# Kernel optimization log

Hardware: AMD Instinct MI355X
Metric: run time of the kernel (lower is better)

Reference implementation:

```python
import jax, jax.numpy as jnp
import numpy as np

C = 64          # channels
K = 15          # sum(shell_sizes)=1+14
H = 32          # neighbors per query
N = 50000       # support points (== query points M)
RADIUS = 1.0
SIGMA = 0.7
INF = 1e6
BN_EPS = 1e-5


def _init_kernel_points(key):
    # stand-in for load_kernels: 1 center point + 14 points on a sphere shell
    pts = jax.random.normal(key, (K - 1, 3), dtype=jnp.float32)
    pts = pts / jnp.linalg.norm(pts, axis=1, keepdims=True) * RADIUS
    return jnp.concatenate([jnp.zeros((1, 3), jnp.float32), pts], axis=0)


def setup_inputs() -> dict:
    key = jax.random.key(0)
    ks = jax.random.split(key, 10)
    q_pts = jax.random.normal(ks[0], (N, 3), dtype=jnp.float32)
    s_pts = jax.random.normal(ks[1], (N, 3), dtype=jnp.float32)
    s_feats = jax.random.normal(ks[2], (N, C), dtype=jnp.float32)
    neighb_inds = jax.random.randint(ks[3], (N, H), 0, N)
    kernel_points = _init_kernel_points(ks[4])
    # alpha_mlp: Linear(C->C, no bias) -> BatchNorm -> LeakyReLU(0.1) -> Linear(C->K*C)
    lim1 = 1.0 / np.sqrt(C)
    W1 = jax.random.uniform(ks[5], (C, C), jnp.float32, -lim1, lim1)
    gamma = jnp.ones((C,), jnp.float32)
    beta = jnp.zeros((C,), jnp.float32)
    W2 = jax.random.uniform(ks[6], (C, K * C), jnp.float32, -lim1, lim1)
    b2 = jax.random.uniform(ks[7], (K * C,), jnp.float32, -lim1, lim1)
    return {"q_pts": q_pts, "s_pts": s_pts, "s_feats": s_feats,
            "neighb_inds": neighb_inds, "kernel_points": kernel_points,
            "W1": W1, "gamma": gamma, "beta": beta, "W2": W2, "b2": b2}


def reference(q_pts, s_pts, s_feats, neighb_inds, kernel_points, W1, gamma, beta, W2, b2):
    M = q_pts.shape[0]
    # alpha_mlp on pooled (= center) features: (M, C) -> (M, K*C)
    h = s_feats @ W1
    mu = jnp.mean(h, axis=0)
    var = jnp.var(h, axis=0)
    h = (h - mu) / jnp.sqrt(var + BN_EPS) * gamma + beta
    h = jax.nn.leaky_relu(h, 0.1)
    conv_weights = (h @ W2 + b2).reshape(M, K, C)

    # gather neighbor features with a zero padding row (index N -> zeros)
    padded_feats = jnp.concatenate([s_feats, jnp.zeros((1, C), s_feats.dtype)], axis=0)
    neighbor_feats = padded_feats[neighb_inds]                 # (M, H, C)

    # relative neighbor positions with inf padding point
    s_pts_pad = jnp.concatenate([s_pts, jnp.full((1, 3), INF, s_pts.dtype)], axis=0)
    neighbors = s_pts_pad[neighb_inds] - q_pts[:, None, :]     # (M, H, 3)

    # kernel-point influence: nearest kernel point + linear influence
    diff = neighbors[:, :, None, :] - kernel_points            # (M, H, K, 3)
    sq_d = jnp.sum(diff * diff, axis=-1)                       # (M, H, K)
    nn_sq = jnp.min(sq_d, axis=-1)                             # (M, H)
    nn_idx = jnp.argmin(sq_d, axis=-1)                         # (M, H)
    infl = jnp.clip(1.0 - jnp.sqrt(nn_sq) / SIGMA, 0.0)        # (M, H)

    # per-neighbor channel weights from the MLP output, gathered by 1nn kernel point
    nw = jnp.take_along_axis(conv_weights, nn_idx[:, :, None], axis=1)  # (M, H, C)
    nw = nw * infl[:, :, None]

    # weighted aggregation (merge=mul, aggr=sum over neighbors)
    return jnp.sum(neighbor_feats * nw, axis=1)                # (M, C)
```

## Files before the change

### kernel.cpp

```cpp
#include <hip/hip_runtime.h>
#include <math.h>

#define N_PTS 50000
#define CCH   64
#define KP    15
#define NH    32
#define SIGMA 0.7f
#define BN_EPS 1e-5f
#define LEAKY 0.1f
#define QB    16
#define STATS_BLOCKS 1024
#define CW_KSTRIDE_B 2176

typedef short bf16x8 __attribute__((ext_vector_type(8)));
typedef float floatx4 __attribute__((ext_vector_type(4)));

__device__ __forceinline__ unsigned short f2b(float f) {
    union { float f; unsigned u; } v; v.f = f;
    return (unsigned short)((v.u + 0x7FFFu + ((v.u >> 16) & 1u)) >> 16);
}
__device__ __forceinline__ float b2f(unsigned short b) {
    union { unsigned u; float f; } v; v.u = ((unsigned)b) << 16;
    return v.f;
}
__device__ __forceinline__ float blo(unsigned u) {
    union { unsigned u; float f; } v; v.u = u << 16;
    return v.f;
}
__device__ __forceinline__ float bhi(unsigned u) {
    union { unsigned u; float f; } v; v.u = u & 0xFFFF0000u;
    return v.f;
}
__device__ __forceinline__ unsigned cvtpk(float lo, float hi) {
    unsigned r;
    asm("v_cvt_pk_bf16_f32 %0, %1, %2" : "=v"(r) : "v"(lo), "v"(hi));
    return r;
}

__global__ __launch_bounds__(256) void k_prep(const float* __restrict__ sf,
                                              const float* __restrict__ W1,
                                              const float* __restrict__ W2,
                                              float* __restrict__ bn,
                                              unsigned short* __restrict__ hst,
                                              unsigned short* __restrict__ w2b,
                                              unsigned short* __restrict__ sfb) {
    int t = threadIdx.x;
    if (blockIdx.x >= STATS_BLOCKS) {
        int g = (blockIdx.x - STATS_BLOCKS) * 256 + t;
        int lane = g & 63, s = (g >> 6) & 1, tt = g >> 7;
        int col = lane & 15, quad = lane >> 4;
        int base = (s * 32 + quad * 8) * 960 + tt * 16 + col;
        ushort4 lo, hi;
        lo.x = f2b(W2[base + 0 * 960]); lo.y = f2b(W2[base + 1 * 960]);
        lo.z = f2b(W2[base + 2 * 960]); lo.w = f2b(W2[base + 3 * 960]);
        hi.x = f2b(W2[base + 4 * 960]); hi.y = f2b(W2[base + 5 * 960]);
        hi.z = f2b(W2[base + 6 * 960]); hi.w = f2b(W2[base + 7 * 960]);
        *(ushort4*)(w2b + g * 8)     = lo;
        *(ushort4*)(w2b + g * 8 + 4) = hi;
        return;
    }
    int c = t & 63, ml = t >> 6;
    float w1c[64];
    #pragma unroll
    for (int i = 0; i < 64; ++i) w1c[i] = W1[i * 64 + c];
    __shared__ float rows[4][64];
    float acc_s = 0.f, acc_q = 0.f;
    for (int m0 = blockIdx.x * 4; m0 < N_PTS; m0 += STATS_BLOCKS * 4) {
        __syncthreads();
        float v = sf[m0 * 64 + t];
        ((float*)rows)[t] = v;
        sfb[m0 * 64 + t] = f2b(v);
        __syncthreads();
        float h = 0.f;
        #pragma unroll
        for (int i4 = 0; i4 < 16; ++i4) {
            float4 r = *(const float4*)&rows[ml][i4 * 4];
            h += r.x * w1c[i4 * 4] + r.y * w1c[i4 * 4 + 1]
               + r.z * w1c[i4 * 4 + 2] + r.w * w1c[i4 * 4 + 3];
        }
        acc_s += h;
        acc_q += h * h;
        hst[(m0 + ml) * 64 + c] = f2b(h);
    }
    __shared__ float red[2][256];
    red[0][t] = acc_s; red[1][t] = acc_q;
    __syncthreads();
    if (t < 64) {
        float s = red[0][t] + red[0][64 + t] + red[0][128 + t] + red[0][192 + t];
        float q = red[1][t] + red[1][64 + t] + red[1][128 + t] + red[1][192 + t];
        atomicAdd(&bn[t], s);
        atomicAdd(&bn[64 + t], q);
    }
}

__global__ __launch_bounds__(256, 4) void k_main(
    const float* __restrict__ q_pts, const float* __restrict__ s_pts,
    const unsigned short* __restrict__ sfb, const int* __restrict__ nb,
    const float* __restrict__ kpts, const float* __restrict__ gamma,
    const float* __restrict__ beta, const float* __restrict__ bn,
    const float* __restrict__ b2, const unsigned short* __restrict__ w2b,
    const unsigned short* __restrict__ hst, float* __restrict__ out) {

    __shared__ __align__(16) unsigned cwP[KP * 32 * 17];
    __shared__ float abS[128];
    __shared__ int      nCnt[QB];
    __shared__ unsigned nPack[QB][NH];
    __shared__ float    nInf[QB][NH];

    int t = threadIdx.x;
    int lane = t & 63, wv = t >> 6;
    int m0 = blockIdx.x * QB;

    if (t < 64) {
        float mu  = bn[t] * (1.0f / N_PTS);
        float var = bn[64 + t] * (1.0f / N_PTS) - mu * mu;
        float a   = gamma[t] * rsqrtf(var + BN_EPS);
        abS[t]      = a;
        abS[64 + t] = beta[t] - mu * a;
    }
    ((unsigned*)nPack)[t]       = 0u;
    ((unsigned*)nPack)[t + 256] = 0u;
    ((float*)nInf)[t]           = 0.f;
    ((float*)nInf)[t + 256]     = 0.f;
    __syncthreads();

    int row = lane & 15, half = lane >> 4;
    bf16x8 r0, r1;
    {
        const unsigned short* hrow = hst + (m0 + row) * 64 + half * 8;
        r0 = *(const bf16x8*)(hrow);
        r1 = *(const bf16x8*)(hrow + 32);
    }

    float kpr[45];
    #pragma unroll
    for (int i = 0; i < 45; ++i) kpr[i] = kpts[i];

    #pragma unroll
    for (int it = 0; it < 2; ++it) {
        int task = t + 256 * it;
        int q = task >> 5, hh = task & 31;
        int m = m0 + q;
        int idx = nb[m * NH + hh];
        float px = s_pts[idx * 3 + 0] - q_pts[m * 3 + 0];
        float py = s_pts[idx * 3 + 1] - q_pts[m * 3 + 1];
        float pz = s_pts[idx * 3 + 2] - q_pts[m * 3 + 2];
        float best = 1e30f; int bi = 0;
        #pragma unroll
        for (int k = 0; k < KP; ++k) {
            float dx = px - kpr[k * 3], dy = py - kpr[k * 3 + 1], dz = pz - kpr[k * 3 + 2];
            float d = dx * dx + dy * dy + dz * dz;
            if (d < best) { best = d; bi = k; }
        }
        float infl = 1.f - sqrtf(best) * (1.0f / SIGMA);
        bool keep = infl > 0.f;
        unsigned long long bal = __ballot(keep);
        unsigned mym = (unsigned)(bal >> (lane & 32));
        int pos = __popc(mym & ((1u << (lane & 31)) - 1u));
        if (keep) {
            nPack[q][pos] = (unsigned)idx | ((unsigned)(bi * CW_KSTRIDE_B) << 16);
            nInf[q][pos]  = infl;
        }
        if ((lane & 31) == 0) nCnt[q] = __popc(mym);
    }

    bf16x8 a0, a1;
    {
        unsigned* A0 = (unsigned*)&a0;
        unsigned* A1 = (unsigned*)&a1;
        #pragma unroll
        for (int jw = 0; jw < 4; ++jw) {
            int c0 = half * 8 + jw * 2;
            float g00 = abS[c0]     * b2f((unsigned short)r0[jw * 2])     + abS[64 + c0];
            float g01 = abS[c0 + 1] * b2f((unsigned short)r0[jw * 2 + 1]) + abS[64 + c0 + 1];
            g00 = g00 > 0.f ? g00 : LEAKY * g00;
            g01 = g01 > 0.f ? g01 : LEAKY * g01;
            A0[jw] = cvtpk(g00, g01);
            int c1 = 32 + c0;
            float g10 = abS[c1]     * b2f((unsigned short)r1[jw * 2])     + abS[64 + c1];
            float g11 = abS[c1 + 1] * b2f((unsigned short)r1[jw * 2 + 1]) + abS[64 + c1 + 1];
            g10 = g10 > 0.f ? g10 : LEAKY * g10;
            g11 = g11 > 0.f ? g11 : LEAKY * g11;
            A1[jw] = cvtpk(g10, g11);
        }
    }

    {
        int colq = lane & 15, quad = lane >> 4;
        bf16x8 Lf[3], Ls[3], Mf[3], Ms[3];
        #pragma unroll
        for (int i = 0; i < 3; ++i) {
            int tt = wv * 15 + i;
            Lf[i] = *(const bf16x8*)(w2b + ((tt * 2 + 0) * 64 + lane) * 8);
            Ls[i] = *(const bf16x8*)(w2b + ((tt * 2 + 1) * 64 + lane) * 8);
        }
        #pragma unroll
        for (int g = 0; g < 5; ++g) {
            if (g < 4) {
                #pragma unroll
                for (int i = 0; i < 3; ++i) {
                    int tt = wv * 15 + (g + 1) * 3 + i;
                    Mf[i] = *(const bf16x8*)(w2b + ((tt * 2 + 0) * 64 + lane) * 8);
                    Ms[i] = *(const bf16x8*)(w2b + ((tt * 2 + 1) * 64 + lane) * 8);
                }
            }
            #pragma unroll
            for (int i = 0; i < 3; ++i) {
                int tt = wv * 15 + g * 3 + i;
                floatx4 acc = {0.f, 0.f, 0.f, 0.f};
                acc = __builtin_amdgcn_mfma_f32_16x16x32_bf16(Lf[i], a0, acc, 0, 0, 0);
                acc = __builtin_amdgcn_mfma_f32_16x16x32_bf16(Ls[i], a1, acc, 0, 0, 0);
                int n0 = tt * 16 + quad * 4;
                float4 bb = *(const float4*)&b2[n0];
                int k  = n0 >> 6;
                int c2 = (n0 & 63) >> 1;
                unsigned w0 = cvtpk(acc[0] + bb.x, acc[1] + bb.y);
                unsigned w1 = cvtpk(acc[2] + bb.z, acc[3] + bb.w);
                unsigned* dst = cwP + (k * 544 + c2 * 17 + colq);
                dst[0]  = w0;
                dst[17] = w1;
            }
            if (g < 4) {
                #pragma unroll
                for (int i = 0; i < 3; ++i) { Lf[i] = Mf[i]; Ls[i] = Ms[i]; }
            }
        }
    }
    __syncthreads();

    {
        int r = lane >> 5, c2 = lane & 31;
        const unsigned short* sfbC = sfb + c2 * 2;
        const unsigned char* cwB = (const unsigned char*)cwP;
        #pragma unroll
        for (int pp = 0; pp < 2; ++pp) {
            int qa = wv * 4 + pp * 2;
            int q  = qa + r;
            const unsigned* packRow = &nPack[q][0];
            const float*    infRow  = &nInf[q][0];
            const unsigned char* cwLane = cwB + (c2 * 17 + q) * 4;
            int nA = nCnt[qa], nB = nCnt[qa + 1];
            int na = nA > nB ? nA : nB;
            float acc0 = 0.f, acc1 = 0.f;
            for (int jj = 0; jj < na; jj += 4) {
                uint4  pk = *(const uint4*)&packRow[jj];
                float4 in = *(const float4*)&infRow[jj];
                unsigned f0 = *(const unsigned*)(sfbC + (pk.x & 0xFFFFu) * 64);
                unsigned f1 = *(const unsigned*)(sfbC + (pk.y & 0xFFFFu) * 64);
                unsigned f2 = *(const unsigned*)(sfbC + (pk.z & 0xFFFFu) * 64);
                unsigned f3 = *(const unsigned*)(sfbC + (pk.w & 0xFFFFu) * 64);
                unsigned w0 = *(const unsigned*)(cwLane + (pk.x >> 16));
                unsigned w1 = *(const unsigned*)(cwLane + (pk.y >> 16));
                unsigned w2 = *(const unsigned*)(cwLane + (pk.z >> 16));
                unsigned w3 = *(const unsigned*)(cwLane + (pk.w >> 16));
                acc0 = fmaf(in.x * blo(f0), blo(w0), acc0);
                acc1 = fmaf(in.x * bhi(f0), bhi(w0), acc1);
                acc0 = fmaf(in.y * blo(f1), blo(w1), acc0);
                acc1 = fmaf(in.y * bhi(f1), bhi(w1), acc1);
                acc0 = fmaf(in.z * blo(f2), blo(w2), acc0);
                acc1 = fmaf(in.z * bhi(f2), bhi(w2), acc1);
                acc0 = fmaf(in.w * blo(f3), blo(w3), acc0);
                acc1 = fmaf(in.w * bhi(f3), bhi(w3), acc1);
            }
            float2 o; o.x = acc0; o.y = acc1;
            *(float2*)&out[(m0 + q) * 64 + c2 * 2] = o;
        }
    }
}

extern "C" void kernel_launch(void* const* d_in, const int* in_sizes, int n_in,
                              void* d_out, int out_size, void* d_ws, size_t ws_size,
                              hipStream_t stream) {
    const float* q_pts   = (const float*)d_in[0];
    const float* s_pts   = (const float*)d_in[1];
    const float* s_feats = (const float*)d_in[2];
    const int*   nb      = (const int*)d_in[3];
    const float* kpts    = (const float*)d_in[4];
    const float* W1      = (const float*)d_in[5];
    const float* gamma   = (const float*)d_in[6];
    const float* beta    = (const float*)d_in[7];
    const float* W2      = (const float*)d_in[8];
    const float* b2      = (const float*)d_in[9];
    float* out = (float*)d_out;

    float* ws = (float*)d_ws;
    float* bn = ws;
    unsigned short* w2b = (unsigned short*)(ws + 128);
    unsigned short* hst = w2b + 61440;
    unsigned short* sfb = hst + N_PTS * CCH;

    hipMemsetAsync(bn, 0, 128 * sizeof(float), stream);
    k_prep<<<STATS_BLOCKS + 30, 256, 0, stream>>>(s_feats, W1, W2, bn, hst, w2b, sfb);
    k_main<<<N_PTS / QB, 256, 0, stream>>>(q_pts, s_pts, sfb, nb, kpts,
                                           gamma, beta, bn, b2, w2b, hst, out);
}
```

Before: 156.4 us.

## Pad support points to float4, hoist neighbor loads, and prefetch gathered feature rows

The prep kernel gains extra blocks that repack s_pts into a 16-byte-aligned float4 array, so the main kernel fetches each neighbor position with one vector load. The main kernel now issues its neighbor-index and point loads before the first barrier, overlapping them with the BN-coefficient setup. It also touches the first words of each kept neighbor's bf16 feature row early to warm the cache before the aggregation phase. This costs an extra 800 KB buffer write, added prep work, and more registers held across the MFMA phase.

```diff
diff --git a/kernel.cpp b/kernel.cpp
--- a/kernel.cpp
+++ b/kernel.cpp
@@ -10,6 +10,7 @@
 #define LEAKY 0.1f
 #define QB    16
 #define STATS_BLOCKS 1024
+#define SP4_BLOCKS 196
 #define CW_KSTRIDE_B 2176
 
 typedef short bf16x8 __attribute__((ext_vector_type(8)));
@@ -40,11 +41,23 @@
 __global__ __launch_bounds__(256) void k_prep(const float* __restrict__ sf,
                                               const float* __restrict__ W1,
                                               const float* __restrict__ W2,
+                                              const float* __restrict__ s_pts,
                                               float* __restrict__ bn,
                                               unsigned short* __restrict__ hst,
                                               unsigned short* __restrict__ w2b,
-                                              unsigned short* __restrict__ sfb) {
+                                              unsigned short* __restrict__ sfb,
+                                              float* __restrict__ sp4) {
     int t = threadIdx.x;
+    if (blockIdx.x >= STATS_BLOCKS + 30) {
+        int g = (blockIdx.x - STATS_BLOCKS - 30) * 256 + t;
+        if (g < N_PTS) {
+            float4 v;
+            v.x = s_pts[g * 3 + 0]; v.y = s_pts[g * 3 + 1];
+            v.z = s_pts[g * 3 + 2]; v.w = 0.f;
+            *(float4*)(sp4 + g * 4) = v;
+        }
+        return;
+    }
     if (blockIdx.x >= STATS_BLOCKS) {
         int g = (blockIdx.x - STATS_BLOCKS) * 256 + t;
         int lane = g & 63, s = (g >> 6) & 1, tt = g >> 7;
@@ -94,7 +107,7 @@
 }
 
 __global__ __launch_bounds__(256, 4) void k_main(
-    const float* __restrict__ q_pts, const float* __restrict__ s_pts,
+    const float* __restrict__ q_pts, const float* __restrict__ sp4,
     const unsigned short* __restrict__ sfb, const int* __restrict__ nb,
     const float* __restrict__ kpts, const float* __restrict__ gamma,
     const float* __restrict__ beta, const float* __restrict__ bn,
@@ -110,6 +123,11 @@
     int t = threadIdx.x;
     int lane = t & 63, wv = t >> 6;
     int m0 = blockIdx.x * QB;
+
+    int q0 = t >> 5, hh = t & 31;
+    int q1 = q0 + 8;
+    int idx0 = nb[(m0 + q0) * NH + hh];
+    int idx1 = nb[(m0 + q1) * NH + hh];
 
     if (t < 64) {
         float mu  = bn[t] * (1.0f / N_PTS);
@@ -122,7 +140,6 @@
     ((unsigned*)nPack)[t + 256] = 0u;
     ((float*)nInf)[t]           = 0.f;
     ((float*)nInf)[t + 256]     = 0.f;
-    __syncthreads();
 
     int row = lane & 15, half = lane >> 4;
     bf16x8 r0, r1;
@@ -132,19 +149,22 @@
         r1 = *(const bf16x8*)(hrow + 32);
     }
 
+    float4 sp0 = *(const float4*)(sp4 + idx0 * 4);
+    float4 sp1 = *(const float4*)(sp4 + idx1 * 4);
+    float qx0 = q_pts[(m0 + q0) * 3 + 0], qy0 = q_pts[(m0 + q0) * 3 + 1],
+          qz0 = q_pts[(m0 + q0) * 3 + 2];
+    float qx1 = q_pts[(m0 + q1) * 3 + 0], qy1 = q_pts[(m0 + q1) * 3 + 1],
+          qz1 = q_pts[(m0 + q1) * 3 + 2];
+
     float kpr[45];
     #pragma unroll
     for (int i = 0; i < 45; ++i) kpr[i] = kpts[i];
 
-    #pragma unroll
-    for (int it = 0; it < 2; ++it) {
-        int task = t + 256 * it;
-        int q = task >> 5, hh = task & 31;
-        int m = m0 + q;
-        int idx = nb[m * NH + hh];
-        float px = s_pts[idx * 3 + 0] - q_pts[m * 3 + 0];
-        float py = s_pts[idx * 3 + 1] - q_pts[m * 3 + 1];
-        float pz = s_pts[idx * 3 + 2] - q_pts[m * 3 + 2];
+    __syncthreads();
+
+    unsigned pf0 = 0, pf1 = 0, pf2 = 0, pf3 = 0;
+    {
+        float px = sp0.x - qx0, py = sp0.y - qy0, pz = sp0.z - qz0;
         float best = 1e30f; int bi = 0;
         #pragma unroll
         for (int k = 0; k < KP; ++k) {
@@ -158,10 +178,34 @@
         unsigned mym = (unsigned)(bal >> (lane & 32));
         int pos = __popc(mym & ((1u << (lane & 31)) - 1u));
         if (keep) {
-            nPack[q][pos] = (unsigned)idx | ((unsigned)(bi * CW_KSTRIDE_B) << 16);
-            nInf[q][pos]  = infl;
-        }
-        if ((lane & 31) == 0) nCnt[q] = __popc(mym);
+            nPack[q0][pos] = (unsigned)idx0 | ((unsigned)(bi * CW_KSTRIDE_B) << 16);
+            nInf[q0][pos]  = infl;
+            const unsigned* rowp = (const unsigned*)(sfb + idx0 * 64);
+            pf0 = rowp[0]; pf1 = rowp[16];
+        }
+        if ((lane & 31) == 0) nCnt[q0] = __popc(mym);
+    }
+    {
+        float px = sp1.x - qx1, py = sp1.y - qy1, pz = sp1.z - qz1;
+        float best = 1e30f; int bi = 0;
+        #pragma unroll
+        for (int k = 0; k < KP; ++k) {
+            float dx = px - kpr[k * 3], dy = py - kpr[k * 3 + 1], dz = pz - kpr[k * 3 + 2];
+            float d = dx * dx + dy * dy + dz * dz;
+            if (d < best) { best = d; bi = k; }
+        }
+        float infl = 1.f - sqrtf(best) * (1.0f / SIGMA);
+        bool keep = infl > 0.f;
+        unsigned long long bal = __ballot(keep);
+        unsigned mym = (unsigned)(bal >> (lane & 32));
+        int pos = __popc(mym & ((1u << (lane & 31)) - 1u));
+        if (keep) {
+            nPack[q1][pos] = (unsigned)idx1 | ((unsigned)(bi * CW_KSTRIDE_B) << 16);
+            nInf[q1][pos]  = infl;
+            const unsigned* rowp = (const unsigned*)(sfb + idx1 * 64);
+            pf2 = rowp[0]; pf3 = rowp[16];
+        }
+        if ((lane & 31) == 0) nCnt[q1] = __popc(mym);
     }
 
     bf16x8 a0, a1;
@@ -226,6 +270,7 @@
             }
         }
     }
+    asm volatile("" :: "v"(pf0), "v"(pf1), "v"(pf2), "v"(pf3));
     __syncthreads();
 
     {
@@ -288,9 +333,11 @@
     unsigned short* w2b = (unsigned short*)(ws + 128);
     unsigned short* hst = w2b + 61440;
     unsigned short* sfb = hst + N_PTS * CCH;
+    float* sp4 = (float*)(sfb + N_PTS * CCH);
 
     hipMemsetAsync(bn, 0, 128 * sizeof(float), stream);
-    k_prep<<<STATS_BLOCKS + 30, 256, 0, stream>>>(s_feats, W1, W2, bn, hst, w2b, sfb);
-    k_main<<<N_PTS / QB, 256, 0, stream>>>(q_pts, s_pts, sfb, nb, kpts,
+    k_prep<<<STATS_BLOCKS + 30 + SP4_BLOCKS, 256, 0, stream>>>(
+        s_feats, W1, W2, s_pts, bn, hst, w2b, sfb, sp4);
+    k_main<<<N_PTS / QB, 256, 0, stream>>>(q_pts, sp4, sfb, nb, kpts,
                                            gamma, beta, bn, b2, w2b, hst, out);
 }
```

Measured after the change: 155.2 us. No clear change (-0.7%).
